# Performance work log

Hardware: AMD Instinct MI355X
Metric: run time of the kernel (lower is better)

## Reference

```python
import jax, jax.numpy as jnp
import numpy as np

DELAY = 8  # init kwarg delay=8


def setup_inputs() -> dict:
    key = jax.random.key(0)
    k1, k2, k3, k4 = jax.random.split(key, 4)
    B, S, F = 64, 2048, 256
    H = 512               # hidden_features (= 2*hf)
    hf = H // 2
    Din = F + 2 + hf      # input_features + 2 (pos enc) + hf
    fn_input = jax.random.normal(k1, (B, S, F), jnp.float32)
    hidden_state = jax.random.normal(k2, (H,), jnp.float32)
    W0 = jax.random.normal(k3, (H, Din), jnp.float32) / np.sqrt(Din).astype(np.float32)
    W1 = jax.random.normal(k4, (H, Din), jnp.float32) / np.sqrt(Din).astype(np.float32)
    return {"fn_input": fn_input, "hidden_state": hidden_state, "W0": W0, "W1": W1}


def _calc(h, s, W):
    # mean-center over the BATCH dim (dim=0 in the torch code)
    out = h - h.mean(axis=0, keepdims=True)
    z = jnp.concatenate([out, s], axis=1) @ W.T      # [B, 2*hf]
    o0, o1 = jnp.split(z, 2, axis=1)
    return jnp.clip(o0, 0.0, 6.0) * jnp.tanh(o1)      # relu6 * tanh gate


def _forward_pass(h, s, W0, W1):
    h0, h1 = jnp.split(h, 2, axis=1)
    o1 = (h1 + _calc(h0, s, W0)) * 0.5                # outputs[1], i=0
    o0 = (h0 + _calc(o1, s, W1)) * 0.5                # outputs[0], i=1
    return jnp.concatenate([o0, o1], axis=1)


def reference(fn_input, hidden_state, W0, W1):
    B, S, F = fn_input.shape
    T = S + DELAY
    # pad with zero inputs for the delay steps
    x_ext = jnp.concatenate([fn_input, jnp.zeros((B, DELAY, F), fn_input.dtype)], axis=1)
    idx = jnp.arange(1, T + 1, dtype=fn_input.dtype)
    factor = jnp.asarray((T + 1) / 2.0, fn_input.dtype)
    pe = jnp.stack([idx, (idx - factor) / factor], axis=-1)  # [T, 2]
    h0 = jnp.broadcast_to(hidden_state[None, :], (B, hidden_state.shape[0]))

    def step(h, xs_t):
        x_t, pe_t = xs_t  # [B, F], [2]
        s = jnp.concatenate(
            [x_t, jnp.broadcast_to(pe_t[None, :], (x_t.shape[0], 2))], axis=1)
        return _forward_pass(h, s, W0, W1), None

    h, _ = jax.lax.scan(step, h0, (jnp.swapaxes(x_ext, 0, 1), pe))
    return h  # [B, 2*hf] (return_sequences=False)
```

## Files before the change

### kernel.cpp

```cpp
#include <hip/hip_runtime.h>


#define T_TOT 2056
#define S_SEQ 2048

typedef _Float16 f16x8 __attribute__((ext_vector_type(8)));
typedef float f32x4 __attribute__((ext_vector_type(4)));

__device__ unsigned long long g_st0[8192];
__device__ unsigned long long g_st1[8192];
__device__ unsigned long long g_pa0[1024];
__device__ unsigned long long g_pa1[1024];

__global__ void init_ws() {
  const int i = (int)blockIdx.x * 256 + (int)threadIdx.x;
  g_st0[i] = 0ull;
  g_st1[i] = 0ull;
  if (i < 1024) { g_pa0[i] = 0ull; g_pa1[i] = 0ull; }
}

#define AL(P) __hip_atomic_load((P), __ATOMIC_RELAXED, __HIP_MEMORY_SCOPE_AGENT)
#define AS(P, V)                                                               \
  __hip_atomic_store((P), (V), __ATOMIC_RELAXED, __HIP_MEMORY_SCOPE_AGENT)

#define PHASE(WS, SIN, PIN, TAGIN, SOUT, POUT, TAGOUT, RAW)                    \
  {                                                                            \
    const unsigned long long* pp_ = (PIN) + 4 * tid;                           \
    const unsigned long long* sp_ =                                            \
        (SIN) + (size_t)(16 * b + n) * 128 + (2 * wv) * 16 + kq * 4;           \
    unsigned long long q0_, q1_, q2_, q3_;                                     \
    unsigned long long s0_, s1_, s2_, s3_, s4_, s5_, s6_, s7_;                 \
    const unsigned tg_ = (unsigned)(TAGIN);                                    \
    int it_ = 0;                                                               \
    for (;;) {                                                                 \
      q0_ = AL(pp_ + 0); q1_ = AL(pp_ + 1);                                    \
      q2_ = AL(pp_ + 2); q3_ = AL(pp_ + 3);                                    \
      s0_ = AL(sp_ + 0); s1_ = AL(sp_ + 1);                                    \
      s2_ = AL(sp_ + 2); s3_ = AL(sp_ + 3);                                    \
      s4_ = AL(sp_ + 16); s5_ = AL(sp_ + 17);                                  \
      s6_ = AL(sp_ + 18); s7_ = AL(sp_ + 19);                                  \
      const unsigned ok_ =                                                     \
          ((unsigned)(q0_ >> 32) >= tg_) & ((unsigned)(q1_ >> 32) >= tg_) &    \
          ((unsigned)(q2_ >> 32) >= tg_) & ((unsigned)(q3_ >> 32) >= tg_) &    \
          ((unsigned)(s0_ >> 32) >= tg_) & ((unsigned)(s1_ >> 32) >= tg_) &    \
          ((unsigned)(s2_ >> 32) >= tg_) & ((unsigned)(s3_ >> 32) >= tg_) &    \
          ((unsigned)(s4_ >> 32) >= tg_) & ((unsigned)(s5_ >> 32) >= tg_) &    \
          ((unsigned)(s6_ >> 32) >= tg_) & ((unsigned)(s7_ >> 32) >= tg_);     \
      if (ok_) break;                                                          \
      if (!alive || ++it_ > (1 << 17)) { alive = 0; break; }                   \
    }                                                                          \
    const float mean_ = (__uint_as_float((unsigned)q0_) +                      \
                         __uint_as_float((unsigned)q1_) +                      \
                         __uint_as_float((unsigned)q2_) +                      \
                         __uint_as_float((unsigned)q3_)) * 0.015625f;          \
    mean_h[tid] = (_Float16)mean_;                                             \
    {                                                                          \
      unsigned long long* lp_ =                                                \
          (unsigned long long*)&lds_s[n][(2 * wv) * 16 + kq * 4];              \
      lp_[0] = ((unsigned long long)(unsigned)s1_ << 32) | (unsigned)s0_;      \
      lp_[1] = ((unsigned long long)(unsigned)s3_ << 32) | (unsigned)s2_;      \
      lp_[8] = ((unsigned long long)(unsigned)s5_ << 32) | (unsigned)s4_;      \
      lp_[9] = ((unsigned long long)(unsigned)s7_ << 32) | (unsigned)s6_;      \
    }                                                                          \
    __syncthreads();                                                           \
    _Pragma("unroll")                                                          \
    for (int kk = 0; kk < 8; ++kk) {                                           \
      const f16x8 sv_ = *(const f16x8*)&lds_s[n][kk * 16 + kq * 4];            \
      const f16x8 mv_ = *(const f16x8*)&mean_h[kk * 32 + kq * 8];              \
      if (kk & 1)                                                              \
        acc1 = __builtin_amdgcn_mfma_f32_16x16x32_f16(sv_ - mv_, (WS)[kk],     \
                                                      acc1, 0, 0, 0);          \
      else                                                                     \
        acc0 = __builtin_amdgcn_mfma_f32_16x16x32_f16(sv_ - mv_, (WS)[kk],     \
                                                      acc0, 0, 0, 0);          \
    }                                                                          \
    float nv_[4], ssum_ = 0.f;                                                 \
    _Pragma("unroll")                                                          \
    for (int r = 0; r < 4; ++r) {                                              \
      const float z = acc0[r] + acc1[r];                                       \
      const float p = __shfl_xor(z, 8);                                        \
      const float z0 = (n < 8) ? z : p;                                        \
      const float z1 = (n < 8) ? p : z;                                        \
       \
      const float z1c = fminf(fmaxf(z1, -10.f), 10.f);                         \
      const float e2 = __expf(2.f * z1c);                                      \
      const float th = (e2 - 1.f) * __builtin_amdgcn_rcpf(e2 + 1.f);           \
      const float cv = fminf(fmaxf(z0, 0.f), 6.f) * th;                        \
      const float o = ((RAW)[r] + cv) * 0.5f;                                  \
      (RAW)[r] = o; nv_[r] = o; ssum_ += o;                                    \
    }                                                                          \
    ssum_ += __shfl_xor(ssum_, 16);                                            \
    ssum_ += __shfl_xor(ssum_, 32);                                            \
    _Pragma("unroll")                                                          \
    for (int r = 0; r < 4; ++r) {                                              \
      union { _Float16 h; unsigned short u; } hb_;                             \
      hb_.h = (_Float16)nv_[r];                                                \
      const unsigned pr_ = (unsigned)__shfl_xor((int)hb_.u, 1) & 0xFFFFu;      \
      if ((n & 1) == 0 && n < 8) {                                             \
        const unsigned dw_ = (unsigned)hb_.u | (pr_ << 16);                    \
        AS((SOUT) + (size_t)(16 * b + kq * 4 + r) * 128 + (ocol >> 1),         \
           ((unsigned long long)(unsigned)(TAGOUT) << 32) |                    \
               (unsigned long long)dw_);                                       \
      }                                                                        \
    }                                                                          \
    if (kq == 0 && n < 8)                                                      \
      AS((POUT) + (size_t)ocol * 4 + b,                                        \
         ((unsigned long long)(unsigned)(TAGOUT) << 32) |                      \
             (unsigned long long)__float_as_uint(ssum_));                      \
    __syncthreads();        \
  }

__launch_bounds__(256, 1)
__global__ void rnn_kernel(const float* __restrict__ xg,
                           const float* __restrict__ hs,
                           const float* __restrict__ W0,
                           const float* __restrict__ W1,
                           float* __restrict__ out) {
  const int wgid = (int)blockIdx.x;
  const int b = wgid & 3;
  const int c = wgid >> 2;
  const int tid = (int)threadIdx.x;
  const int wv = tid >> 6;
  const int ln = tid & 63;
  const int n = ln & 15;
  const int kq = ln >> 4;
  const int ocol = c * 32 + wv * 8 + (n & 7);
  const int wrow = (n < 8) ? ocol : (256 + ocol);

  __shared__ __align__(16) unsigned lds_s[16][132];
  __shared__ __align__(16) _Float16 mean_h[256];

  f16x8 w0s[8], w0x[8], w1s[8], w1x[8];
  float w0pa, w0pb, w1pa, w1pb;
  {
    const float* r0 = W0 + (size_t)wrow * 514;
    const float* r1 = W1 + (size_t)wrow * 514;
#pragma unroll
    for (int kk = 0; kk < 8; ++kk) {
      const int k0 = kk * 32 + kq * 8;
      f16x8 a, bx, a1, bx1;
#pragma unroll
      for (int j = 0; j < 8; ++j) {
        a[j]   = (_Float16)r0[k0 + j];
        bx[j]  = (_Float16)r0[256 + k0 + j];
        a1[j]  = (_Float16)r1[k0 + j];
        bx1[j] = (_Float16)r1[256 + k0 + j];
      }
      w0s[kk] = a; w0x[kk] = bx; w1s[kk] = a1; w1x[kk] = bx1;
    }
    w0pa = r0[512]; w0pb = r0[513];
    w1pa = r1[512]; w1pb = r1[513];
  }

  float raw0[4], raw1[4];
#pragma unroll
  for (int r = 0; r < 4; ++r) { raw0[r] = hs[ocol]; raw1[r] = hs[256 + ocol]; }

  int alive = 1;

  {
    union { _Float16 h; unsigned short u; } e0, e1;
    e0.h = (_Float16)hs[ocol]; e1.h = (_Float16)hs[ocol + 1];
    const unsigned dw = (unsigned)e0.u | ((unsigned)e1.u << 16);
    if ((n & 1) == 0 && n < 8) {
#pragma unroll
      for (int r = 0; r < 4; ++r)
        AS(g_st0 + (size_t)(16 * b + kq * 4 + r) * 128 + (ocol >> 1),
           (1ull << 32) | (unsigned long long)dw);
    }
    if (kq == 0 && n < 8)
      AS(g_pa0 + (size_t)ocol * 4 + b,
         (1ull << 32) |
             (unsigned long long)__float_as_uint(16.f * hs[ocol]));
  }

  f32x4 xf[16];
  f16x8 xa[8];
  const int arow = 16 * b + n;
  {
    const float* xp = xg + (size_t)arow * S_SEQ * 256 + kq * 8;
#pragma unroll
    for (int kk = 0; kk < 8; ++kk) {
      xf[2 * kk]     = *(const f32x4*)(xp + kk * 32);
      xf[2 * kk + 1] = *(const f32x4*)(xp + kk * 32 + 4);
    }
  }

  for (int t = 0; t < T_TOT; ++t) {
    const float pe0 = (float)(t + 1);
    const float pe1 = (pe0 - 1028.5f) * (1.0f / 1028.5f);
    const int have_x = (t < S_SEQ);

    {
      f32x4 acc0, acc1;
      const float pt = pe0 * w0pa + pe1 * w0pb;
      acc0[0] = pt; acc0[1] = pt; acc0[2] = pt; acc0[3] = pt;
      acc1[0] = 0.f; acc1[1] = 0.f; acc1[2] = 0.f; acc1[3] = 0.f;
      if (have_x) {
#pragma unroll
        for (int kk = 0; kk < 8; ++kk) {
          f16x8 af;
#pragma unroll
          for (int j = 0; j < 4; ++j) {
            af[j]     = (_Float16)xf[2 * kk][j];
            af[4 + j] = (_Float16)xf[2 * kk + 1][j];
          }
          xa[kk] = af;
          if (kk & 1)
            acc1 = __builtin_amdgcn_mfma_f32_16x16x32_f16(af, w0x[kk], acc1,
                                                          0, 0, 0);
          else
            acc0 = __builtin_amdgcn_mfma_f32_16x16x32_f16(af, w0x[kk], acc0,
                                                          0, 0, 0);
        }
      }
      PHASE(w0s, g_st0, g_pa0, 2 * t + 1, g_st1, g_pa1, 2 * t + 2, raw1);
    }

    {
      f32x4 acc0, acc1;
      const float pt = pe0 * w1pa + pe1 * w1pb;
      acc0[0] = pt; acc0[1] = pt; acc0[2] = pt; acc0[3] = pt;
      acc1[0] = 0.f; acc1[1] = 0.f; acc1[2] = 0.f; acc1[3] = 0.f;
      if (have_x) {
#pragma unroll
        for (int kk = 0; kk < 8; ++kk) {
          if (kk & 1)
            acc1 = __builtin_amdgcn_mfma_f32_16x16x32_f16(xa[kk], w1x[kk],
                                                          acc1, 0, 0, 0);
          else
            acc0 = __builtin_amdgcn_mfma_f32_16x16x32_f16(xa[kk], w1x[kk],
                                                          acc0, 0, 0, 0);
        }
      }
      if (t + 1 < S_SEQ) {
        const float* xp = xg + ((size_t)arow * S_SEQ + (t + 1)) * 256 + kq * 8;
#pragma unroll
        for (int kk = 0; kk < 8; ++kk) {
          xf[2 * kk]     = *(const f32x4*)(xp + kk * 32);
          xf[2 * kk + 1] = *(const f32x4*)(xp + kk * 32 + 4);
        }
      }
      PHASE(w1s, g_st1, g_pa1, 2 * t + 2, g_st0, g_pa0, 2 * t + 3, raw0);
    }
  }

  if (n < 8) {
#pragma unroll
    for (int r = 0; r < 4; ++r) {
      const int row = 16 * b + kq * 4 + r;
      out[(size_t)row * 512 + ocol] = raw0[r];
      out[(size_t)row * 512 + 256 + ocol] = raw1[r];
    }
  }
}

#undef PHASE
#undef AS
#undef AL

extern "C" void kernel_launch(void* const* d_in, const int* in_sizes, int n_in,
                              void* d_out, int out_size, void* d_ws, size_t ws_size,
                              hipStream_t stream) {
  (void)in_sizes; (void)n_in; (void)out_size; (void)d_ws; (void)ws_size;
  const float* x  = (const float*)d_in[0];
  const float* hs = (const float*)d_in[1];
  const float* W0 = (const float*)d_in[2];
  const float* W1 = (const float*)d_in[3];
  float* out = (float*)d_out;

  init_ws<<<dim3(32), dim3(256), 0, stream>>>();
  rnn_kernel<<<dim3(32), dim3(256), 0, stream>>>(x, hs, W0, W1, out);
}
```

Before: 14.76 ms.

## Issue spin-wait loads before x MFMAs and stage x via async global-to-LDS

Splits each phase's spin-wait so the first poll of the neighbour state and partial-sum flags is issued before the input-projection MFMAs, hiding that load latency behind compute. Moves input prefetch from register-held f32 vectors to a double-buffered LDS tile filled with global_load_lds, issued one step ahead. This frees many VGPRs and overlaps the x fetch with the recurrence. In exchange it adds an explicit vmcnt wait before publishing state and relies on the phase syncthreads to order LDS buffer reuse.

```diff
diff --git a/kernel.cpp b/kernel.cpp
--- a/kernel.cpp
+++ b/kernel.cpp
@@ -23,22 +23,23 @@
 #define AS(P, V)                                                               \
   __hip_atomic_store((P), (V), __ATOMIC_RELAXED, __HIP_MEMORY_SCOPE_AGENT)
 
-#define PHASE(WS, SIN, PIN, TAGIN, SOUT, POUT, TAGOUT, RAW)                    \
-  {                                                                            \
+#define PHASE_BEGIN(SIN, PIN)                                                  \
     const unsigned long long* pp_ = (PIN) + 4 * tid;                           \
     const unsigned long long* sp_ =                                            \
         (SIN) + (size_t)(16 * b + n) * 128 + (2 * wv) * 16 + kq * 4;           \
-    unsigned long long q0_, q1_, q2_, q3_;                                     \
-    unsigned long long s0_, s1_, s2_, s3_, s4_, s5_, s6_, s7_;                 \
+    unsigned long long q0_ = AL(pp_ + 0), q1_ = AL(pp_ + 1),                   \
+                       q2_ = AL(pp_ + 2), q3_ = AL(pp_ + 3);                   \
+    unsigned long long s0_ = AL(sp_ + 0), s1_ = AL(sp_ + 1),                   \
+                       s2_ = AL(sp_ + 2), s3_ = AL(sp_ + 3),                   \
+                       s4_ = AL(sp_ + 16), s5_ = AL(sp_ + 17),                 \
+                       s6_ = AL(sp_ + 18), s7_ = AL(sp_ + 19);                 \
+    asm volatile("" ::: "memory");
+
+#define PHASE_END(TAGIN, WS, SOUT, POUT, TAGOUT, RAW, DO_VM)                   \
+  {                                                                            \
     const unsigned tg_ = (unsigned)(TAGIN);                                    \
     int it_ = 0;                                                               \
     for (;;) {                                                                 \
-      q0_ = AL(pp_ + 0); q1_ = AL(pp_ + 1);                                    \
-      q2_ = AL(pp_ + 2); q3_ = AL(pp_ + 3);                                    \
-      s0_ = AL(sp_ + 0); s1_ = AL(sp_ + 1);                                    \
-      s2_ = AL(sp_ + 2); s3_ = AL(sp_ + 3);                                    \
-      s4_ = AL(sp_ + 16); s5_ = AL(sp_ + 17);                                  \
-      s6_ = AL(sp_ + 18); s7_ = AL(sp_ + 19);                                  \
       const unsigned ok_ =                                                     \
           ((unsigned)(q0_ >> 32) >= tg_) & ((unsigned)(q1_ >> 32) >= tg_) &    \
           ((unsigned)(q2_ >> 32) >= tg_) & ((unsigned)(q3_ >> 32) >= tg_) &    \
@@ -48,6 +49,12 @@
           ((unsigned)(s6_ >> 32) >= tg_) & ((unsigned)(s7_ >> 32) >= tg_);     \
       if (ok_) break;                                                          \
       if (!alive || ++it_ > (1 << 17)) { alive = 0; break; }                   \
+      q0_ = AL(pp_ + 0); q1_ = AL(pp_ + 1);                                    \
+      q2_ = AL(pp_ + 2); q3_ = AL(pp_ + 3);                                    \
+      s0_ = AL(sp_ + 0); s1_ = AL(sp_ + 1);                                    \
+      s2_ = AL(sp_ + 2); s3_ = AL(sp_ + 3);                                    \
+      s4_ = AL(sp_ + 16); s5_ = AL(sp_ + 17);                                  \
+      s6_ = AL(sp_ + 18); s7_ = AL(sp_ + 19);                                  \
     }                                                                          \
     const float mean_ = (__uint_as_float((unsigned)q0_) +                      \
                          __uint_as_float((unsigned)q1_) +                      \
@@ -91,6 +98,8 @@
     }                                                                          \
     ssum_ += __shfl_xor(ssum_, 16);                                            \
     ssum_ += __shfl_xor(ssum_, 32);                                            \
+    if (DO_VM)    \
+      asm volatile("s_waitcnt vmcnt(0)" ::: "memory");                         \
     _Pragma("unroll")                                                          \
     for (int r = 0; r < 4; ++r) {                                              \
       union { _Float16 h; unsigned short u; } hb_;                             \
@@ -107,7 +116,22 @@
       AS((POUT) + (size_t)ocol * 4 + b,                                        \
          ((unsigned long long)(unsigned)(TAGOUT) << 32) |                      \
              (unsigned long long)__float_as_uint(ssum_));                      \
-    __syncthreads();        \
+    __syncthreads();              \
+  }
+
+#define STAGE_X(TT)                                                            \
+  if ((TT) < S_SEQ) {                                                          \
+    const int bf_ = (TT) & 1;                                                  \
+    _Pragma("unroll")                                                          \
+    for (int j_ = 0; j_ < 4; ++j_) {                                           \
+      const int row_ = wv * 4 + j_;                                            \
+      const float* gs_ =                                                       \
+          xg + ((size_t)(16 * b + row_) * S_SEQ + (TT)) * 256 + ln * 4;        \
+      __builtin_amdgcn_global_load_lds(                                        \
+          (const __attribute__((address_space(1))) unsigned*)gs_,              \
+          (__attribute__((address_space(3))) unsigned*)&xs[bf_][row_][0],      \
+          16, 0, 0);                                                           \
+    }                                                                          \
   }
 
 __launch_bounds__(256, 1)
@@ -129,6 +153,7 @@
 
   __shared__ __align__(16) unsigned lds_s[16][132];
   __shared__ __align__(16) _Float16 mean_h[256];
+  __shared__ __align__(16) float xs[2][16][262];
 
   f16x8 w0s[8], w0x[8], w1s[8], w1x[8];
   float w0pa, w0pb, w1pa, w1pb;
@@ -174,18 +199,11 @@
              (unsigned long long)__float_as_uint(16.f * hs[ocol]));
   }
 
-  f32x4 xf[16];
+  STAGE_X(0);
+  asm volatile("s_waitcnt vmcnt(0)" ::: "memory");
+  __syncthreads();
+
   f16x8 xa[8];
-  const int arow = 16 * b + n;
-  {
-    const float* xp = xg + (size_t)arow * S_SEQ * 256 + kq * 8;
-#pragma unroll
-    for (int kk = 0; kk < 8; ++kk) {
-      xf[2 * kk]     = *(const f32x4*)(xp + kk * 32);
-      xf[2 * kk + 1] = *(const f32x4*)(xp + kk * 32 + 4);
-    }
-  }
-
   for (int t = 0; t < T_TOT; ++t) {
     const float pe0 = (float)(t + 1);
     const float pe1 = (pe0 - 1028.5f) * (1.0f / 1028.5f);
@@ -196,15 +214,21 @@
       const float pt = pe0 * w0pa + pe1 * w0pb;
       acc0[0] = pt; acc0[1] = pt; acc0[2] = pt; acc0[3] = pt;
       acc1[0] = 0.f; acc1[1] = 0.f; acc1[2] = 0.f; acc1[3] = 0.f;
+      PHASE_BEGIN(g_st0, g_pa0);
+      STAGE_X(t + 1);
       if (have_x) {
+        const float* xr = &xs[t & 1][n][0];
 #pragma unroll
         for (int kk = 0; kk < 8; ++kk) {
+          const float2 a0 = *(const float2*)(xr + kk * 32 + kq * 8);
+          const float2 a1 = *(const float2*)(xr + kk * 32 + kq * 8 + 2);
+          const float2 a2 = *(const float2*)(xr + kk * 32 + kq * 8 + 4);
+          const float2 a3 = *(const float2*)(xr + kk * 32 + kq * 8 + 6);
           f16x8 af;
-#pragma unroll
-          for (int j = 0; j < 4; ++j) {
-            af[j]     = (_Float16)xf[2 * kk][j];
-            af[4 + j] = (_Float16)xf[2 * kk + 1][j];
-          }
+          af[0] = (_Float16)a0.x; af[1] = (_Float16)a0.y;
+          af[2] = (_Float16)a1.x; af[3] = (_Float16)a1.y;
+          af[4] = (_Float16)a2.x; af[5] = (_Float16)a2.y;
+          af[6] = (_Float16)a3.x; af[7] = (_Float16)a3.y;
           xa[kk] = af;
           if (kk & 1)
             acc1 = __builtin_amdgcn_mfma_f32_16x16x32_f16(af, w0x[kk], acc1,
@@ -214,7 +238,7 @@
                                                           0, 0, 0);
         }
       }
-      PHASE(w0s, g_st0, g_pa0, 2 * t + 1, g_st1, g_pa1, 2 * t + 2, raw1);
+      PHASE_END(2 * t + 1, w0s, g_st1, g_pa1, 2 * t + 2, raw1, 1);
     }
 
     {
@@ -222,6 +246,7 @@
       const float pt = pe0 * w1pa + pe1 * w1pb;
       acc0[0] = pt; acc0[1] = pt; acc0[2] = pt; acc0[3] = pt;
       acc1[0] = 0.f; acc1[1] = 0.f; acc1[2] = 0.f; acc1[3] = 0.f;
+      PHASE_BEGIN(g_st1, g_pa1);
       if (have_x) {
 #pragma unroll
         for (int kk = 0; kk < 8; ++kk) {
@@ -233,15 +258,7 @@
                                                           acc0, 0, 0, 0);
         }
       }
-      if (t + 1 < S_SEQ) {
-        const float* xp = xg + ((size_t)arow * S_SEQ + (t + 1)) * 256 + kq * 8;
-#pragma unroll
-        for (int kk = 0; kk < 8; ++kk) {
-          xf[2 * kk]     = *(const f32x4*)(xp + kk * 32);
-          xf[2 * kk + 1] = *(const f32x4*)(xp + kk * 32 + 4);
-        }
-      }
-      PHASE(w1s, g_st1, g_pa1, 2 * t + 2, g_st0, g_pa0, 2 * t + 3, raw0);
+      PHASE_END(2 * t + 2, w1s, g_st0, g_pa0, 2 * t + 3, raw0, 0);
     }
   }
 
@@ -255,7 +272,9 @@
   }
 }
 
-#undef PHASE
+#undef STAGE_X
+#undef PHASE_END
+#undef PHASE_BEGIN
 #undef AS
 #undef AL
 
```

New measurement: 16.37 ms. +11.0%, slower.

## Halve block count by giving each wave two output column groups; poll only stale flags

Applied to the files above, without the earlier changes.

Each wave now computes two groups of 8 output columns instead of one, so the grid shrinks from 32 to 16 blocks. This halves the number of blocks taking part in the per-step cross-block flag synchronization. The spin-wait also loads all flags once up front and then reloads only the ones whose tag is still stale, with a lower timeout bound. In exchange each wave holds twice the weight registers and does twice the MFMA and epilogue work per step, which may raise register pressure and lengthen the serial critical path.

```diff
diff --git a/kernel.cpp b/kernel.cpp
--- a/kernel.cpp
+++ b/kernel.cpp
@@ -23,31 +23,40 @@
 #define AS(P, V)                                                               \
   __hip_atomic_store((P), (V), __ATOMIC_RELAXED, __HIP_MEMORY_SCOPE_AGENT)
 
-#define PHASE(WS, SIN, PIN, TAGIN, SOUT, POUT, TAGOUT, RAW)                    \
+#define TAGOK(Q) ((unsigned)((Q) >> 32) >= tg_)
+
+#define PHASE(SIN, PIN, TAGIN, WS, SOUT, POUT, TAGOUT, RAW)                    \
   {                                                                            \
     const unsigned long long* pp_ = (PIN) + 4 * tid;                           \
     const unsigned long long* sp_ =                                            \
         (SIN) + (size_t)(16 * b + n) * 128 + (2 * wv) * 16 + kq * 4;           \
-    unsigned long long q0_, q1_, q2_, q3_;                                     \
-    unsigned long long s0_, s1_, s2_, s3_, s4_, s5_, s6_, s7_;                 \
     const unsigned tg_ = (unsigned)(TAGIN);                                    \
+    unsigned long long q0_ = AL(pp_ + 0), q1_ = AL(pp_ + 1),                   \
+                       q2_ = AL(pp_ + 2), q3_ = AL(pp_ + 3);                   \
+    unsigned long long s0_ = AL(sp_ + 0), s1_ = AL(sp_ + 1),                   \
+                       s2_ = AL(sp_ + 2), s3_ = AL(sp_ + 3),                   \
+                       s4_ = AL(sp_ + 16), s5_ = AL(sp_ + 17),                 \
+                       s6_ = AL(sp_ + 18), s7_ = AL(sp_ + 19);                 \
     int it_ = 0;                                                               \
     for (;;) {                                                                 \
-      q0_ = AL(pp_ + 0); q1_ = AL(pp_ + 1);                                    \
-      q2_ = AL(pp_ + 2); q3_ = AL(pp_ + 3);                                    \
-      s0_ = AL(sp_ + 0); s1_ = AL(sp_ + 1);                                    \
-      s2_ = AL(sp_ + 2); s3_ = AL(sp_ + 3);                                    \
-      s4_ = AL(sp_ + 16); s5_ = AL(sp_ + 17);                                  \
-      s6_ = AL(sp_ + 18); s7_ = AL(sp_ + 19);                                  \
-      const unsigned ok_ =                                                     \
-          ((unsigned)(q0_ >> 32) >= tg_) & ((unsigned)(q1_ >> 32) >= tg_) &    \
-          ((unsigned)(q2_ >> 32) >= tg_) & ((unsigned)(q3_ >> 32) >= tg_) &    \
-          ((unsigned)(s0_ >> 32) >= tg_) & ((unsigned)(s1_ >> 32) >= tg_) &    \
-          ((unsigned)(s2_ >> 32) >= tg_) & ((unsigned)(s3_ >> 32) >= tg_) &    \
-          ((unsigned)(s4_ >> 32) >= tg_) & ((unsigned)(s5_ >> 32) >= tg_) &    \
-          ((unsigned)(s6_ >> 32) >= tg_) & ((unsigned)(s7_ >> 32) >= tg_);     \
-      if (ok_) break;                                                          \
-      if (!alive || ++it_ > (1 << 17)) { alive = 0; break; }                   \
+      if (TAGOK(q0_) && TAGOK(q1_) && TAGOK(q2_) && TAGOK(q3_) &&              \
+          TAGOK(s0_) && TAGOK(s1_) && TAGOK(s2_) && TAGOK(s3_) &&              \
+          TAGOK(s4_) && TAGOK(s5_) && TAGOK(s6_) && TAGOK(s7_))                \
+        break;                                                                 \
+      if (!alive || ++it_ > (1 << 16)) { alive = 0; break; }                   \
+          \
+      if (!TAGOK(q0_)) q0_ = AL(pp_ + 0);                                      \
+      if (!TAGOK(q1_)) q1_ = AL(pp_ + 1);                                      \
+      if (!TAGOK(q2_)) q2_ = AL(pp_ + 2);                                      \
+      if (!TAGOK(q3_)) q3_ = AL(pp_ + 3);                                      \
+      if (!TAGOK(s0_)) s0_ = AL(sp_ + 0);                                      \
+      if (!TAGOK(s1_)) s1_ = AL(sp_ + 1);                                      \
+      if (!TAGOK(s2_)) s2_ = AL(sp_ + 2);                                      \
+      if (!TAGOK(s3_)) s3_ = AL(sp_ + 3);                                      \
+      if (!TAGOK(s4_)) s4_ = AL(sp_ + 16);                                     \
+      if (!TAGOK(s5_)) s5_ = AL(sp_ + 17);                                     \
+      if (!TAGOK(s6_)) s6_ = AL(sp_ + 18);                                     \
+      if (!TAGOK(s7_)) s7_ = AL(sp_ + 19);                                     \
     }                                                                          \
     const float mean_ = (__uint_as_float((unsigned)q0_) +                      \
                          __uint_as_float((unsigned)q1_) +                      \
@@ -67,46 +76,53 @@
     for (int kk = 0; kk < 8; ++kk) {                                           \
       const f16x8 sv_ = *(const f16x8*)&lds_s[n][kk * 16 + kq * 4];            \
       const f16x8 mv_ = *(const f16x8*)&mean_h[kk * 32 + kq * 8];              \
-      if (kk & 1)                                                              \
-        acc1 = __builtin_amdgcn_mfma_f32_16x16x32_f16(sv_ - mv_, (WS)[kk],     \
-                                                      acc1, 0, 0, 0);          \
-      else                                                                     \
-        acc0 = __builtin_amdgcn_mfma_f32_16x16x32_f16(sv_ - mv_, (WS)[kk],     \
-                                                      acc0, 0, 0, 0);          \
-    }                                                                          \
-    float nv_[4], ssum_ = 0.f;                                                 \
-    _Pragma("unroll")                                                          \
-    for (int r = 0; r < 4; ++r) {                                              \
-      const float z = acc0[r] + acc1[r];                                       \
-      const float p = __shfl_xor(z, 8);                                        \
-      const float z0 = (n < 8) ? z : p;                                        \
-      const float z1 = (n < 8) ? p : z;                                        \
-       \
-      const float z1c = fminf(fmaxf(z1, -10.f), 10.f);                         \
-      const float e2 = __expf(2.f * z1c);                                      \
-      const float th = (e2 - 1.f) * __builtin_amdgcn_rcpf(e2 + 1.f);           \
-      const float cv = fminf(fmaxf(z0, 0.f), 6.f) * th;                        \
-      const float o = ((RAW)[r] + cv) * 0.5f;                                  \
-      (RAW)[r] = o; nv_[r] = o; ssum_ += o;                                    \
-    }                                                                          \
-    ssum_ += __shfl_xor(ssum_, 16);                                            \
-    ssum_ += __shfl_xor(ssum_, 32);                                            \
-    _Pragma("unroll")                                                          \
-    for (int r = 0; r < 4; ++r) {                                              \
-      union { _Float16 h; unsigned short u; } hb_;                             \
-      hb_.h = (_Float16)nv_[r];                                                \
-      const unsigned pr_ = (unsigned)__shfl_xor((int)hb_.u, 1) & 0xFFFFu;      \
-      if ((n & 1) == 0 && n < 8) {                                             \
-        const unsigned dw_ = (unsigned)hb_.u | (pr_ << 16);                    \
-        AS((SOUT) + (size_t)(16 * b + kq * 4 + r) * 128 + (ocol >> 1),         \
-           ((unsigned long long)(unsigned)(TAGOUT) << 32) |                    \
-               (unsigned long long)dw_);                                       \
+      const f16x8 av_ = sv_ - mv_;                                             \
+      _Pragma("unroll")                                                        \
+      for (int g = 0; g < 2; ++g) {                                            \
+        if (kk & 1)                                                            \
+          acc1[g] = __builtin_amdgcn_mfma_f32_16x16x32_f16(av_, (WS)[g][kk],   \
+                                                           acc1[g], 0, 0, 0); \
+        else                                                                   \
+          acc0[g] = __builtin_amdgcn_mfma_f32_16x16x32_f16(av_, (WS)[g][kk],   \
+                                                           acc0[g], 0, 0, 0); \
       }                                                                        \
     }                                                                          \
-    if (kq == 0 && n < 8)                                                      \
-      AS((POUT) + (size_t)ocol * 4 + b,                                        \
-         ((unsigned long long)(unsigned)(TAGOUT) << 32) |                      \
-             (unsigned long long)__float_as_uint(ssum_));                      \
+    _Pragma("unroll")                                                          \
+    for (int g = 0; g < 2; ++g) {                                              \
+      float nv_[4], ssum_ = 0.f;                                               \
+      _Pragma("unroll")                                                        \
+      for (int r = 0; r < 4; ++r) {                                            \
+        const float z = acc0[g][r] + acc1[g][r];                               \
+        const float p = __shfl_xor(z, 8);                                      \
+        const float z0 = (n < 8) ? z : p;                                      \
+        const float z1 = (n < 8) ? p : z;                                      \
+        const float z1c = fminf(fmaxf(z1, -10.f), 10.f);                       \
+        const float e2 = __expf(2.f * z1c);                                    \
+        const float th = (e2 - 1.f) * __builtin_amdgcn_rcpf(e2 + 1.f);         \
+        const float cv = fminf(fmaxf(z0, 0.f), 6.f) * th;                      \
+        const float o = ((RAW)[g][r] + cv) * 0.5f;                             \
+        (RAW)[g][r] = o; nv_[r] = o; ssum_ += o;                               \
+      }                                                                        \
+      ssum_ += __shfl_xor(ssum_, 16);                                          \
+      ssum_ += __shfl_xor(ssum_, 32);                                          \
+      const int ocg_ = ocol0 + g * 8;                                          \
+      _Pragma("unroll")                                                        \
+      for (int r = 0; r < 4; ++r) {                                            \
+        union { _Float16 h; unsigned short u; } hb_;                           \
+        hb_.h = (_Float16)nv_[r];                                              \
+        const unsigned pr_ = (unsigned)__shfl_xor((int)hb_.u, 1) & 0xFFFFu;    \
+        if ((n & 1) == 0 && n < 8) {                                           \
+          const unsigned dw_ = (unsigned)hb_.u | (pr_ << 16);                  \
+          AS((SOUT) + (size_t)(16 * b + kq * 4 + r) * 128 + (ocg_ >> 1),       \
+             ((unsigned long long)(unsigned)(TAGOUT) << 32) |                  \
+                 (unsigned long long)dw_);                                     \
+        }                                                                      \
+      }                                                                        \
+      if (kq == 0 && n < 8)                                                    \
+        AS((POUT) + (size_t)ocg_ * 4 + b,                                      \
+           ((unsigned long long)(unsigned)(TAGOUT) << 32) |                    \
+               (unsigned long long)__float_as_uint(ssum_));                    \
+    }                                                                          \
     __syncthreads();        \
   }
 
@@ -124,15 +140,17 @@
   const int ln = tid & 63;
   const int n = ln & 15;
   const int kq = ln >> 4;
-  const int ocol = c * 32 + wv * 8 + (n & 7);
-  const int wrow = (n < 8) ? ocol : (256 + ocol);
+  const int ocol0 = c * 64 + wv * 16 + (n & 7);
 
   __shared__ __align__(16) unsigned lds_s[16][132];
   __shared__ __align__(16) _Float16 mean_h[256];
 
-  f16x8 w0s[8], w0x[8], w1s[8], w1x[8];
-  float w0pa, w0pb, w1pa, w1pb;
-  {
+  f16x8 w0s[2][8], w0x[2][8], w1s[2][8], w1x[2][8];
+  float w0pa[2], w0pb[2], w1pa[2], w1pb[2];
+#pragma unroll
+  for (int g = 0; g < 2; ++g) {
+    const int ocg = ocol0 + g * 8;
+    const int wrow = (n < 8) ? ocg : (256 + ocg);
     const float* r0 = W0 + (size_t)wrow * 514;
     const float* r1 = W1 + (size_t)wrow * 514;
 #pragma unroll
@@ -146,32 +164,38 @@
         a1[j]  = (_Float16)r1[k0 + j];
         bx1[j] = (_Float16)r1[256 + k0 + j];
       }
-      w0s[kk] = a; w0x[kk] = bx; w1s[kk] = a1; w1x[kk] = bx1;
-    }
-    w0pa = r0[512]; w0pb = r0[513];
-    w1pa = r1[512]; w1pb = r1[513];
-  }
-
-  float raw0[4], raw1[4];
-#pragma unroll
-  for (int r = 0; r < 4; ++r) { raw0[r] = hs[ocol]; raw1[r] = hs[256 + ocol]; }
+      w0s[g][kk] = a; w0x[g][kk] = bx; w1s[g][kk] = a1; w1x[g][kk] = bx1;
+    }
+    w0pa[g] = r0[512]; w0pb[g] = r0[513];
+    w1pa[g] = r1[512]; w1pb[g] = r1[513];
+  }
+
+  float raw0[2][4], raw1[2][4];
+#pragma unroll
+  for (int g = 0; g < 2; ++g)
+#pragma unroll
+    for (int r = 0; r < 4; ++r) {
+      raw0[g][r] = hs[ocol0 + g * 8];
+      raw1[g][r] = hs[256 + ocol0 + g * 8];
+    }
 
   int alive = 1;
 
-  {
+#pragma unroll
+  for (int g = 0; g < 2; ++g) {
+    const int ocg = ocol0 + g * 8;
     union { _Float16 h; unsigned short u; } e0, e1;
-    e0.h = (_Float16)hs[ocol]; e1.h = (_Float16)hs[ocol + 1];
+    e0.h = (_Float16)hs[ocg]; e1.h = (_Float16)hs[ocg + 1];
     const unsigned dw = (unsigned)e0.u | ((unsigned)e1.u << 16);
     if ((n & 1) == 0 && n < 8) {
 #pragma unroll
       for (int r = 0; r < 4; ++r)
-        AS(g_st0 + (size_t)(16 * b + kq * 4 + r) * 128 + (ocol >> 1),
+        AS(g_st0 + (size_t)(16 * b + kq * 4 + r) * 128 + (ocg >> 1),
            (1ull << 32) | (unsigned long long)dw);
     }
     if (kq == 0 && n < 8)
-      AS(g_pa0 + (size_t)ocol * 4 + b,
-         (1ull << 32) |
-             (unsigned long long)__float_as_uint(16.f * hs[ocol]));
+      AS(g_pa0 + (size_t)ocg * 4 + b,
+         (1ull << 32) | (unsigned long long)__float_as_uint(16.f * hs[ocg]));
   }
 
   f32x4 xf[16];
@@ -192,10 +216,13 @@
     const int have_x = (t < S_SEQ);
 
     {
-      f32x4 acc0, acc1;
-      const float pt = pe0 * w0pa + pe1 * w0pb;
-      acc0[0] = pt; acc0[1] = pt; acc0[2] = pt; acc0[3] = pt;
-      acc1[0] = 0.f; acc1[1] = 0.f; acc1[2] = 0.f; acc1[3] = 0.f;
+      f32x4 acc0[2], acc1[2];
+#pragma unroll
+      for (int g = 0; g < 2; ++g) {
+        const float pt = pe0 * w0pa[g] + pe1 * w0pb[g];
+        acc0[g][0] = pt; acc0[g][1] = pt; acc0[g][2] = pt; acc0[g][3] = pt;
+        acc1[g][0] = 0.f; acc1[g][1] = 0.f; acc1[g][2] = 0.f; acc1[g][3] = 0.f;
+      }
       if (have_x) {
 #pragma unroll
         for (int kk = 0; kk < 8; ++kk) {
@@ -206,31 +233,42 @@
             af[4 + j] = (_Float16)xf[2 * kk + 1][j];
           }
           xa[kk] = af;
-          if (kk & 1)
-            acc1 = __builtin_amdgcn_mfma_f32_16x16x32_f16(af, w0x[kk], acc1,
-                                                          0, 0, 0);
-          else
-            acc0 = __builtin_amdgcn_mfma_f32_16x16x32_f16(af, w0x[kk], acc0,
-                                                          0, 0, 0);
+#pragma unroll
+          for (int g = 0; g < 2; ++g) {
+            if (kk & 1)
+              acc1[g] = __builtin_amdgcn_mfma_f32_16x16x32_f16(af, w0x[g][kk],
+                                                               acc1[g], 0, 0, 0);
+            else
+              acc0[g] = __builtin_amdgcn_mfma_f32_16x16x32_f16(af, w0x[g][kk],
+                                                               acc0[g], 0, 0, 0);
+          }
         }
       }
-      PHASE(w0s, g_st0, g_pa0, 2 * t + 1, g_st1, g_pa1, 2 * t + 2, raw1);
+      PHASE(g_st0, g_pa0, 2 * t + 1, w0s, g_st1, g_pa1, 2 * t + 2, raw1);
     }
 
     {
-      f32x4 acc0, acc1;
-      const float pt = pe0 * w1pa + pe1 * w1pb;
-      acc0[0] = pt; acc0[1] = pt; acc0[2] = pt; acc0[3] = pt;
-      acc1[0] = 0.f; acc1[1] = 0.f; acc1[2] = 0.f; acc1[3] = 0.f;
+      f32x4 acc0[2], acc1[2];
+#pragma unroll
+      for (int g = 0; g < 2; ++g) {
+        const float pt = pe0 * w1pa[g] + pe1 * w1pb[g];
+        acc0[g][0] = pt; acc0[g][1] = pt; acc0[g][2] = pt; acc0[g][3] = pt;
+        acc1[g][0] = 0.f; acc1[g][1] = 0.f; acc1[g][2] = 0.f; acc1[g][3] = 0.f;
+      }
       if (have_x) {
 #pragma unroll
         for (int kk = 0; kk < 8; ++kk) {
-          if (kk & 1)
-            acc1 = __builtin_amdgcn_mfma_f32_16x16x32_f16(xa[kk], w1x[kk],
-                                                          acc1, 0, 0, 0);
-          else
-            acc0 = __builtin_amdgcn_mfma_f32_16x16x32_f16(xa[kk], w1x[kk],
-                                                          acc0, 0, 0, 0);
+#pragma unroll
+          for (int g = 0; g < 2; ++g) {
+            if (kk & 1)
+              acc1[g] = __builtin_amdgcn_mfma_f32_16x16x32_f16(xa[kk],
+                                                               w1x[g][kk],
+                                                               acc1[g], 0, 0, 0);
+            else
+              acc0[g] = __builtin_amdgcn_mfma_f32_16x16x32_f16(xa[kk],
+                                                               w1x[g][kk],
+                                                               acc0[g], 0, 0, 0);
+          }
         }
       }
       if (t + 1 < S_SEQ) {
@@ -241,21 +279,24 @@
           xf[2 * kk + 1] = *(const f32x4*)(xp + kk * 32 + 4);
         }
       }
-      PHASE(w1s, g_st1, g_pa1, 2 * t + 2, g_st0, g_pa0, 2 * t + 3, raw0);
+      PHASE(g_st1, g_pa1, 2 * t + 2, w1s, g_st0, g_pa0, 2 * t + 3, raw0);
     }
   }
 
   if (n < 8) {
 #pragma unroll
-    for (int r = 0; r < 4; ++r) {
-      const int row = 16 * b + kq * 4 + r;
-      out[(size_t)row * 512 + ocol] = raw0[r];
-      out[(size_t)row * 512 + 256 + ocol] = raw1[r];
-    }
+    for (int g = 0; g < 2; ++g)
+#pragma unroll
+      for (int r = 0; r < 4; ++r) {
+        const int row = 16 * b + kq * 4 + r;
+        out[(size_t)row * 512 + ocol0 + g * 8] = raw0[g][r];
+        out[(size_t)row * 512 + 256 + ocol0 + g * 8] = raw1[g][r];
+      }
   }
 }
 
 #undef PHASE
+#undef TAGOK
 #undef AS
 #undef AL
 
@@ -270,5 +311,5 @@
   float* out = (float*)d_out;
 
   init_ws<<<dim3(32), dim3(256), 0, stream>>>();
-  rnn_kernel<<<dim3(32), dim3(256), 0, stream>>>(x, hs, W0, W1, out);
+  rnn_kernel<<<dim3(16), dim3(256), 0, stream>>>(x, hs, W0, W1, out);
 }
```

After: 20.47 ms. 38.7% more time.

## Co-locate workgroups on one XCD and switch to per-producer flag handshakes

Applied to the files above, without the earlier changes.

Launches 1024 workgroups and lets the first 32 that land on the same XCD (read from the hardware XCC_ID register) claim the recurrence roles, so cross-workgroup traffic stays within one die's L2. The other workgroups exit at once. Per-element tagged polling is replaced by per-workgroup ready flags: one wave polls 12 producer flags with atomic ops while the other waves spin on an LDS go-tag. The data is then read with non-temporal loads, and each element is re-checked only if its tag is stale. Stores become atomic swaps. The risks are extra launch overhead and relying on enough workgroups reaching a single XCD; if fewer than 32 do, the spin timeouts mark the kernel dead and the results are wrong.

```diff
diff --git a/kernel.cpp b/kernel.cpp
--- a/kernel.cpp
+++ b/kernel.cpp
@@ -11,44 +11,88 @@
 __device__ unsigned long long g_st1[8192];
 __device__ unsigned long long g_pa0[1024];
 __device__ unsigned long long g_pa1[1024];
+__device__ unsigned g_fl[2][32];
+__device__ unsigned g_ctrl[2];
 
 __global__ void init_ws() {
   const int i = (int)blockIdx.x * 256 + (int)threadIdx.x;
   g_st0[i] = 0ull;
   g_st1[i] = 0ull;
   if (i < 1024) { g_pa0[i] = 0ull; g_pa1[i] = 0ull; }
+  if (i < 64) g_fl[i >> 5][i & 31] = 0u;
+  if (i < 2) g_ctrl[i] = 0u;
 }
 
-#define AL(P) __hip_atomic_load((P), __ATOMIC_RELAXED, __HIP_MEMORY_SCOPE_AGENT)
-#define AS(P, V)                                                               \
-  __hip_atomic_store((P), (V), __ATOMIC_RELAXED, __HIP_MEMORY_SCOPE_AGENT)
+#define ASWAP64(P, V)                                                          \
+  asm volatile("global_atomic_swap_x2 %0, %1, off"                             \
+               :: "v"((void*)(P)), "v"((unsigned long long)(V)) : "memory")
+#define ASWAP32(P, V)                                                          \
+  asm volatile("global_atomic_swap %0, %1, off"                                \
+               :: "v"((void*)(P)), "v"((unsigned)(V)) : "memory")
+
+#define CHK(W, P)                                                              \
+  {                                                                            \
+    int itc_ = 0;                                                              \
+    while ((unsigned)((W) >> 32) < tg_) {                                      \
+      if (!alive || ++itc_ > (1 << 16)) { alive = 0; break; }                  \
+      unsigned long long zz_ = 0ull, rr_;                                      \
+      asm volatile("global_atomic_or_x2 %0, %1, %2, off sc0\n\t"               \
+                   "s_waitcnt vmcnt(0)"                                        \
+                   : "=&v"(rr_) : "v"((void*)(P)), "v"(zz_) : "memory");       \
+      (W) = rr_;                                                               \
+    }                                                                          \
+  }
 
 #define PHASE(WS, SIN, PIN, TAGIN, SOUT, POUT, TAGOUT, RAW)                    \
   {                                                                            \
+    const unsigned tg_ = (unsigned)(TAGIN);                                    \
+    if (wv == 0) {                                                             \
+      if (ln < 12) {                                                           \
+        const int prod_ = (ln < 4) ? (4 * c + ln) : (4 * (ln - 4) + b);        \
+        unsigned* fp_ = &g_fl[tg_ & 1][prod_];                                 \
+        int it_ = 0;                                                           \
+        for (;;) {                                                             \
+          unsigned fv_, z32_ = 0u;                                             \
+          asm volatile("global_atomic_or %0, %1, %2, off sc0\n\t"              \
+                       "s_waitcnt vmcnt(0)"                                    \
+                       : "=&v"(fv_) : "v"((void*)fp_), "v"(z32_) : "memory");  \
+          if (fv_ >= tg_) break;                                               \
+          if (!alive || ++it_ > (1 << 17)) { alive = 0; break; }               \
+        }                                                                      \
+      }                                                                        \
+      if (ln == 0) *gop = tg_;                                                 \
+    } else {                                                                   \
+      int it_ = 0;                                                             \
+      while (*gop < tg_) {                                                     \
+        if (!alive || ++it_ > (1 << 18)) { alive = 0; break; }                 \
+      }                                                                        \
+    }                                                                          \
     const unsigned long long* pp_ = (PIN) + 4 * tid;                           \
     const unsigned long long* sp_ =                                            \
         (SIN) + (size_t)(16 * b + n) * 128 + (2 * wv) * 16 + kq * 4;           \
     unsigned long long q0_, q1_, q2_, q3_;                                     \
     unsigned long long s0_, s1_, s2_, s3_, s4_, s5_, s6_, s7_;                 \
-    const unsigned tg_ = (unsigned)(TAGIN);                                    \
-    int it_ = 0;                                                               \
-    for (;;) {                                                                 \
-      q0_ = AL(pp_ + 0); q1_ = AL(pp_ + 1);                                    \
-      q2_ = AL(pp_ + 2); q3_ = AL(pp_ + 3);                                    \
-      s0_ = AL(sp_ + 0); s1_ = AL(sp_ + 1);                                    \
-      s2_ = AL(sp_ + 2); s3_ = AL(sp_ + 3);                                    \
-      s4_ = AL(sp_ + 16); s5_ = AL(sp_ + 17);                                  \
-      s6_ = AL(sp_ + 18); s7_ = AL(sp_ + 19);                                  \
-      const unsigned ok_ =                                                     \
-          ((unsigned)(q0_ >> 32) >= tg_) & ((unsigned)(q1_ >> 32) >= tg_) &    \
-          ((unsigned)(q2_ >> 32) >= tg_) & ((unsigned)(q3_ >> 32) >= tg_) &    \
-          ((unsigned)(s0_ >> 32) >= tg_) & ((unsigned)(s1_ >> 32) >= tg_) &    \
-          ((unsigned)(s2_ >> 32) >= tg_) & ((unsigned)(s3_ >> 32) >= tg_) &    \
-          ((unsigned)(s4_ >> 32) >= tg_) & ((unsigned)(s5_ >> 32) >= tg_) &    \
-          ((unsigned)(s6_ >> 32) >= tg_) & ((unsigned)(s7_ >> 32) >= tg_);     \
-      if (ok_) break;                                                          \
-      if (!alive || ++it_ > (1 << 17)) { alive = 0; break; }                   \
-    }                                                                          \
+    asm volatile("global_load_dwordx2 %0, %12, off sc0 nt\n\t"                 \
+                 "global_load_dwordx2 %1, %12, off offset:8 sc0 nt\n\t"        \
+                 "global_load_dwordx2 %2, %12, off offset:16 sc0 nt\n\t"       \
+                 "global_load_dwordx2 %3, %12, off offset:24 sc0 nt\n\t"       \
+                 "global_load_dwordx2 %4, %13, off sc0 nt\n\t"                 \
+                 "global_load_dwordx2 %5, %13, off offset:8 sc0 nt\n\t"        \
+                 "global_load_dwordx2 %6, %13, off offset:16 sc0 nt\n\t"       \
+                 "global_load_dwordx2 %7, %13, off offset:24 sc0 nt\n\t"       \
+                 "global_load_dwordx2 %8, %13, off offset:128 sc0 nt\n\t"      \
+                 "global_load_dwordx2 %9, %13, off offset:136 sc0 nt\n\t"      \
+                 "global_load_dwordx2 %10, %13, off offset:144 sc0 nt\n\t"     \
+                 "global_load_dwordx2 %11, %13, off offset:152 sc0 nt\n\t"     \
+                 "s_waitcnt vmcnt(0)"                                          \
+                 : "=&v"(q0_), "=&v"(q1_), "=&v"(q2_), "=&v"(q3_),             \
+                   "=&v"(s0_), "=&v"(s1_), "=&v"(s2_), "=&v"(s3_),             \
+                   "=&v"(s4_), "=&v"(s5_), "=&v"(s6_), "=&v"(s7_)              \
+                 : "v"(pp_), "v"(sp_) : "memory");                             \
+    CHK(q0_, pp_ + 0) CHK(q1_, pp_ + 1) CHK(q2_, pp_ + 2) CHK(q3_, pp_ + 3)    \
+    CHK(s0_, sp_ + 0) CHK(s1_, sp_ + 1) CHK(s2_, sp_ + 2) CHK(s3_, sp_ + 3)    \
+    CHK(s4_, sp_ + 16) CHK(s5_, sp_ + 17) CHK(s6_, sp_ + 18)                   \
+    CHK(s7_, sp_ + 19)                                                         \
     const float mean_ = (__uint_as_float((unsigned)q0_) +                      \
                          __uint_as_float((unsigned)q1_) +                      \
                          __uint_as_float((unsigned)q2_) +                      \
@@ -98,16 +142,18 @@
       const unsigned pr_ = (unsigned)__shfl_xor((int)hb_.u, 1) & 0xFFFFu;      \
       if ((n & 1) == 0 && n < 8) {                                             \
         const unsigned dw_ = (unsigned)hb_.u | (pr_ << 16);                    \
-        AS((SOUT) + (size_t)(16 * b + kq * 4 + r) * 128 + (ocol >> 1),         \
-           ((unsigned long long)(unsigned)(TAGOUT) << 32) |                    \
-               (unsigned long long)dw_);                                       \
+        ASWAP64((SOUT) + (size_t)(16 * b + kq * 4 + r) * 128 + (ocol >> 1),    \
+                ((unsigned long long)(unsigned)(TAGOUT) << 32) |               \
+                    (unsigned long long)dw_);                                  \
       }                                                                        \
     }                                                                          \
     if (kq == 0 && n < 8)                                                      \
-      AS((POUT) + (size_t)ocol * 4 + b,                                        \
-         ((unsigned long long)(unsigned)(TAGOUT) << 32) |                      \
-             (unsigned long long)__float_as_uint(ssum_));                      \
+      ASWAP64((POUT) + (size_t)ocol * 4 + b,                                   \
+              ((unsigned long long)(unsigned)(TAGOUT) << 32) |                 \
+                  (unsigned long long)__float_as_uint(ssum_));                 \
     __syncthreads();        \
+    if (tid == 0) ASWAP32(&g_fl[(unsigned)(TAGOUT) & 1][wg],                   \
+                          (unsigned)(TAGOUT));                                 \
   }
 
 __launch_bounds__(256, 1)
@@ -116,16 +162,37 @@
                            const float* __restrict__ W0,
                            const float* __restrict__ W1,
                            float* __restrict__ out) {
-  const int wgid = (int)blockIdx.x;
-  const int b = wgid & 3;
-  const int c = wgid >> 2;
   const int tid = (int)threadIdx.x;
+  __shared__ int role_sh;
+  __shared__ volatile unsigned go_tag;
+
+  if (tid == 0) {
+    unsigned xcd;
+    asm volatile("s_getreg_b32 %0, hwreg(HW_REG_XCC_ID)" : "=s"(xcd));
+    const unsigned me = xcd + 1u;
+    const unsigned prev = atomicCAS(&g_ctrl[0], 0u, me);
+    const unsigned tgt = (prev == 0u) ? me : prev;
+    int role = -1;
+    if (me == tgt) {
+      const unsigned tk = atomicAdd(&g_ctrl[1], 1u);
+      if (tk < 32u) role = (int)tk;
+    }
+    role_sh = role;
+    go_tag = 0u;
+  }
+  __syncthreads();
+  const int wg = role_sh;
+  if (wg < 0) return;
+
+  const int b = wg & 3;
+  const int c = wg >> 2;
   const int wv = tid >> 6;
   const int ln = tid & 63;
   const int n = ln & 15;
   const int kq = ln >> 4;
   const int ocol = c * 32 + wv * 8 + (n & 7);
   const int wrow = (n < 8) ? ocol : (256 + ocol);
+  volatile unsigned* gop = &go_tag;
 
   __shared__ __align__(16) unsigned lds_s[16][132];
   __shared__ __align__(16) _Float16 mean_h[256];
@@ -165,14 +232,16 @@
     if ((n & 1) == 0 && n < 8) {
 #pragma unroll
       for (int r = 0; r < 4; ++r)
-        AS(g_st0 + (size_t)(16 * b + kq * 4 + r) * 128 + (ocol >> 1),
-           (1ull << 32) | (unsigned long long)dw);
+        ASWAP64(g_st0 + (size_t)(16 * b + kq * 4 + r) * 128 + (ocol >> 1),
+                (1ull << 32) | (unsigned long long)dw);
     }
     if (kq == 0 && n < 8)
-      AS(g_pa0 + (size_t)ocol * 4 + b,
-         (1ull << 32) |
-             (unsigned long long)__float_as_uint(16.f * hs[ocol]));
-  }
+      ASWAP64(g_pa0 + (size_t)ocol * 4 + b,
+              (1ull << 32) |
+                  (unsigned long long)__float_as_uint(16.f * hs[ocol]));
+  }
+  __syncthreads();
+  if (tid == 0) ASWAP32(&g_fl[1][wg], 1u);
 
   f32x4 xf[16];
   f16x8 xa[8];
@@ -256,8 +325,9 @@
 }
 
 #undef PHASE
-#undef AS
-#undef AL
+#undef CHK
+#undef ASWAP32
+#undef ASWAP64
 
 extern "C" void kernel_launch(void* const* d_in, const int* in_sizes, int n_in,
                               void* d_out, int out_size, void* d_ws, size_t ws_size,
@@ -270,5 +340,5 @@
   float* out = (float*)d_out;
 
   init_ws<<<dim3(32), dim3(256), 0, stream>>>();
-  rnn_kernel<<<dim3(32), dim3(256), 0, stream>>>(x, hs, W0, W1, out);
+  rnn_kernel<<<dim3(1024), dim3(256), 0, stream>>>(x, hs, W0, W1, out);
 }
```

After: 20.12 ms. 1.36x slower.
